# Performance work log

Measured on AMD Instinct MI355X. Metric: run time of the kernel, lower is better.

The kernel has to match this reference:

```python
import jax, jax.numpy as jnp
import numpy as np

SIGMA_INIT = 1000.0


def setup_inputs() -> dict:
    key = jax.random.key(0)
    k1, k2, k3 = jax.random.split(key, 3)
    B, M, D, S = 1024, 209, 12288, 2
    input_data = jax.random.normal(k1, (B, D), dtype=jnp.float32)
    center = jax.random.normal(k2, (M, D), dtype=jnp.float32)
    sigma = SIGMA_INIT * jnp.ones((M,), dtype=jnp.float32)
    W = 50.0 * jax.random.normal(k3, (S, M), dtype=jnp.float32)
    b = jnp.zeros((S,), dtype=jnp.float32)
    return {"input_data": input_data, "center": center, "sigma": sigma, "W": W, "b": b}


def reference(input_data, center, sigma, W, b):
    # Euclidean distance ||x_i - c_j|| via GEMM expansion (avoids [B,M,D] diff tensor)
    x2 = jnp.sum(input_data * input_data, axis=1, keepdims=True)        # [B,1]
    c2 = jnp.sum(center * center, axis=1)[None, :]                      # [1,M]
    d2 = x2 + c2 - 2.0 * (input_data @ center.T)                        # [B,M]
    dist = jnp.sqrt(jnp.maximum(d2, 0.0))
    # Note: original divides the (non-squared) norm by sigma^2, then exp(-.)
    radial = jnp.exp(-dist / (sigma * sigma)[None, :])                  # [B,M]
    return radial @ W.T + b                                             # [B,S]
```

## Files before the change

### kernel.cpp

```cpp
#include <hip/hip_runtime.h>
#include <hip/hip_bf16.h>
#include <stdint.h>

#define B_SZ 1024
#define M_SZ 209
#define MPAD 224
#define D_SZ 12288
#define KC   48
#define KCH  (D_SZ / KC)
#define BK   64
#define NIT  (KCH / BK)
#define NB   16
#define BT   64
#define NCT  14

#define CBF_OFF  0u
#define XXP_OFF  (MPAD * D_SZ * 2)
#define CC_OFF   (XXP_OFF + B_SZ * KC * 4)
#define SLAB_OFF (CC_OFF + 1024)

typedef __attribute__((ext_vector_type(8))) short short8;
typedef __attribute__((ext_vector_type(4))) float floatx4;

__device__ __forceinline__ uint32_t pk2(float lo, float hi) {
    union { __hip_bfloat162 h; uint32_t u; } cv;
    cv.h = __float22bfloat162_rn(float2{lo, hi});
    return cv.u;
}

__device__ __forceinline__ void gload_lds16(const void* g, void* l) {
    __builtin_amdgcn_global_load_lds(
        (const __attribute__((address_space(1))) void*)g,
        (__attribute__((address_space(3))) void*)l, 16, 0, 0);
}

__global__ __launch_bounds__(256) void rbf_prep(
    const float* __restrict__ c, unsigned short* __restrict__ cbf,
    float* __restrict__ cc)
{
    __shared__ float red[4];
    const int j = blockIdx.x, t = threadIdx.x;
    unsigned short* dst = cbf + (size_t)j * D_SZ;
    float s = 0.f;
    if (j < M_SZ) {
        const float* src = c + (size_t)j * D_SZ;
        for (int i = t * 4; i < D_SZ; i += 1024) {
            float4 v = *(const float4*)(src + i);
            s += v.x*v.x + v.y*v.y + v.z*v.z + v.w*v.w;
            uint2 w = { pk2(v.x, v.y), pk2(v.z, v.w) };
            *(uint2*)(dst + i) = w;
        }
    } else {
        uint2 zz = {0u, 0u};
        for (int i = t * 4; i < D_SZ; i += 1024) *(uint2*)(dst + i) = zz;
    }
#pragma unroll
    for (int off = 32; off > 0; off >>= 1) s += __shfl_down(s, off);
    if ((t & 63) == 0) red[t >> 6] = s;
    __syncthreads();
    if (t == 0 && j < M_SZ) cc[j] = red[0] + red[1] + red[2] + red[3];
}

__global__ __launch_bounds__(256, 3) void rbf_main(
    const float* __restrict__ x, const unsigned short* __restrict__ cbf,
    __hip_bfloat16* __restrict__ slab, float* __restrict__ xxp)
{
    __shared__ unsigned short sx[BT * BK];
    __shared__ unsigned short sc[MPAD * BK];

    const int t    = threadIdx.x;
    const int k    = blockIdx.x;
    const int b    = blockIdx.y;
    const int wave = t >> 6, lane = t & 63;
    const int quad = lane >> 4, mrow = lane & 15;
    const int m3   = mrow & 7;

    floatx4 acc[NCT];
    const floatx4 z4 = {0.f, 0.f, 0.f, 0.f};
#pragma unroll
    for (int i = 0; i < NCT; ++i) acc[i] = z4;

    const int r  = t >> 2;
    const int c0 = (t & 3) * 2;
    const float* xp = x + (size_t)(b * BT + r) * D_SZ + (size_t)k * KCH + (t & 3) * 16;
    unsigned short* xw0 = &sx[r * BK + ((c0    ) ^ (r & 7)) * 8];
    unsigned short* xw1 = &sx[r * BK + ((c0 + 1) ^ (r & 7)) * 8];

    const int lr8 = lane >> 3, lc8 = lane & 7;
    const unsigned short* cpb = cbf + (size_t)lr8 * D_SZ + (size_t)k * KCH
                              + (size_t)((lc8 ^ lr8) * 8);

    const unsigned short* ax0 = &sx[(wave * 16 + mrow) * BK + ((quad    ) ^ m3) * 8];
    const unsigned short* ax1 = &sx[(wave * 16 + mrow) * BK + ((quad + 4) ^ m3) * 8];
    const unsigned short* bx0 = &sc[mrow * BK + ((quad    ) ^ m3) * 8];
    const unsigned short* bx1 = &sc[mrow * BK + ((quad + 4) ^ m3) * 8];

    float sxx = 0.f;

    for (int it = 0; it < NIT; ++it) {
#pragma unroll
        for (int j = 0; j < 7; ++j) {
            const int cr = wave * 7 + j;
            gload_lds16(cpb + (size_t)cr * 8 * D_SZ + it * BK, &sc[cr * 512]);
        }
        {
            float4 v0 = *(const float4*)(xp + 0);
            float4 v1 = *(const float4*)(xp + 4);
            float4 v2 = *(const float4*)(xp + 8);
            float4 v3 = *(const float4*)(xp + 12);
            sxx += v0.x*v0.x + v0.y*v0.y + v0.z*v0.z + v0.w*v0.w
                 + v1.x*v1.x + v1.y*v1.y + v1.z*v1.z + v1.w*v1.w
                 + v2.x*v2.x + v2.y*v2.y + v2.z*v2.z + v2.w*v2.w
                 + v3.x*v3.x + v3.y*v3.y + v3.z*v3.z + v3.w*v3.w;
            uint4 w0 = { pk2(v0.x,v0.y), pk2(v0.z,v0.w), pk2(v1.x,v1.y), pk2(v1.z,v1.w) };
            uint4 w1 = { pk2(v2.x,v2.y), pk2(v2.z,v2.w), pk2(v3.x,v3.y), pk2(v3.z,v3.w) };
            *(uint4*)xw0 = w0;
            *(uint4*)xw1 = w1;
        }
        __syncthreads();

#pragma unroll
        for (int ks = 0; ks < 2; ++ks) {
            short8 a = *(const short8*)(ks ? ax1 : ax0);
            const unsigned short* bb = ks ? bx1 : bx0;
#pragma unroll
            for (int ct = 0; ct < NCT; ++ct) {
                short8 bf = *(const short8*)(bb + ct * 1024);
                acc[ct] = __builtin_amdgcn_mfma_f32_16x16x32_bf16(a, bf, acc[ct], 0, 0, 0);
            }
        }
        __syncthreads();
        xp += BK;
    }

    __hip_bfloat16* sd = slab + (size_t)k * B_SZ * M_SZ;
    const int gi0 = b * BT + wave * 16 + quad * 4;
#pragma unroll
    for (int ct = 0; ct < NCT; ++ct) {
        const int gj = ct * 16 + mrow;
        if (gj < M_SZ) {
#pragma unroll
            for (int rg = 0; rg < 4; ++rg)
                sd[(size_t)(gi0 + rg) * M_SZ + gj] = __float2bfloat16(acc[ct][rg]);
        }
    }

    sxx += __shfl_down(sxx, 2);
    sxx += __shfl_down(sxx, 1);
    if ((t & 3) == 0) xxp[(size_t)(b * BT + r) * KC + k] = sxx;
}

__global__ __launch_bounds__(256) void rbf_fin(
    const __hip_bfloat16* __restrict__ slab, const float* __restrict__ xxp,
    const float* __restrict__ cc, const float* __restrict__ sigma,
    const float* __restrict__ W, const float* __restrict__ bias,
    float* __restrict__ out)
{
    const int wave = threadIdx.x >> 6, lane = threadIdx.x & 63;
    const int i = blockIdx.x * 4 + wave;

    float xv = (lane < KC) ? xxp[(size_t)i * KC + lane] : 0.f;
#pragma unroll
    for (int off = 32; off > 0; off >>= 1) xv += __shfl_down(xv, off);
    const float xxi = __shfl(xv, 0);

    float a0 = 0.f, a1 = 0.f;
    for (int j = lane; j < M_SZ; j += 64) {
        float s = 0.f;
#pragma unroll
        for (int kk = 0; kk < KC; ++kk)
            s += __bfloat162float(slab[(size_t)kk * B_SZ * M_SZ + (size_t)i * M_SZ + j]);
        float d2 = fmaxf(xxi + cc[j] - 2.f * s, 0.f);
        float sg = sigma[j];
        float rad = __expf(-sqrtf(d2) / (sg * sg));
        a0 += rad * W[j];
        a1 += rad * W[M_SZ + j];
    }
#pragma unroll
    for (int off = 32; off > 0; off >>= 1) {
        a0 += __shfl_down(a0, off);
        a1 += __shfl_down(a1, off);
    }
    if (lane == 0) {
        out[i * 2 + 0] = a0 + bias[0];
        out[i * 2 + 1] = a1 + bias[1];
    }
}

extern "C" void kernel_launch(void* const* d_in, const int* in_sizes, int n_in,
                              void* d_out, int out_size, void* d_ws, size_t ws_size,
                              hipStream_t stream)
{
    const float* x     = (const float*)d_in[0];
    const float* c     = (const float*)d_in[1];
    const float* sigma = (const float*)d_in[2];
    const float* W     = (const float*)d_in[3];
    const float* bias  = (const float*)d_in[4];
    float* out = (float*)d_out;

    char* ws = (char*)d_ws;
    unsigned short*  cbf  = (unsigned short*)(ws + CBF_OFF);
    float*           xxp  = (float*)(ws + XXP_OFF);
    float*           cc   = (float*)(ws + CC_OFF);
    __hip_bfloat16*  slab = (__hip_bfloat16*)(ws + SLAB_OFF);

    rbf_prep<<<MPAD, 256, 0, stream>>>(c, cbf, cc);
    rbf_main<<<dim3(KC, NB), 256, 0, stream>>>(x, cbf, slab, xxp);
    rbf_fin<<<B_SZ / 4, 256, 0, stream>>>(slab, xxp, cc, sigma, W, bias, out);
}
```

Baseline: 119.1 us.

## Relayout partial-sum slab per row and vectorize split-K reduction

The split-K partial slab is stored so that each row's 48 partial chunks sit together (row stride KC*256), which lets the final kernel read 16-byte vectors and reduce across K in a block-per-row layout with shared-memory partials. The main kernel now prefetches all of its x tile (4 iterations) into registers before the K loop, so global load latency no longer stalls inside the loop. The prep kernel switches to 16-byte stores. The cost is higher register pressure in the main kernel and a slab that includes the padded columns.

```diff
diff --git a/kernel.cpp b/kernel.cpp
--- a/kernel.cpp
+++ b/kernel.cpp
@@ -13,6 +13,8 @@
 #define NB   16
 #define BT   64
 #define NCT  14
+#define SROW 256
+#define SLROW (KC * SROW)
 
 #define CBF_OFF  0u
 #define XXP_OFF  (MPAD * D_SZ * 2)
@@ -26,6 +28,12 @@
     union { __hip_bfloat162 h; uint32_t u; } cv;
     cv.h = __float22bfloat162_rn(float2{lo, hi});
     return cv.u;
+}
+
+__device__ __forceinline__ float bfbits2f(unsigned short u) {
+    union { uint32_t u; float f; } cv;
+    cv.u = ((uint32_t)u) << 16;
+    return cv.f;
 }
 
 __device__ __forceinline__ void gload_lds16(const void* g, void* l) {
@@ -44,15 +52,17 @@
     float s = 0.f;
     if (j < M_SZ) {
         const float* src = c + (size_t)j * D_SZ;
-        for (int i = t * 4; i < D_SZ; i += 1024) {
-            float4 v = *(const float4*)(src + i);
-            s += v.x*v.x + v.y*v.y + v.z*v.z + v.w*v.w;
-            uint2 w = { pk2(v.x, v.y), pk2(v.z, v.w) };
-            *(uint2*)(dst + i) = w;
+        for (int i = t * 8; i < D_SZ; i += 2048) {
+            float4 v0 = *(const float4*)(src + i);
+            float4 v1 = *(const float4*)(src + i + 4);
+            s += v0.x*v0.x + v0.y*v0.y + v0.z*v0.z + v0.w*v0.w
+               + v1.x*v1.x + v1.y*v1.y + v1.z*v1.z + v1.w*v1.w;
+            uint4 w = { pk2(v0.x,v0.y), pk2(v0.z,v0.w), pk2(v1.x,v1.y), pk2(v1.z,v1.w) };
+            *(uint4*)(dst + i) = w;
         }
     } else {
-        uint2 zz = {0u, 0u};
-        for (int i = t * 4; i < D_SZ; i += 1024) *(uint2*)(dst + i) = zz;
+        uint4 zz = {0u, 0u, 0u, 0u};
+        for (int i = t * 8; i < D_SZ; i += 2048) *(uint4*)(dst + i) = zz;
     }
 #pragma unroll
     for (int off = 32; off > 0; off >>= 1) s += __shfl_down(s, off);
@@ -83,6 +93,23 @@
     const int r  = t >> 2;
     const int c0 = (t & 3) * 2;
     const float* xp = x + (size_t)(b * BT + r) * D_SZ + (size_t)k * KCH + (t & 3) * 16;
+
+    uint4 xw[NIT][2];
+    float sxx = 0.f;
+#pragma unroll
+    for (int it = 0; it < NIT; ++it) {
+        float4 v0 = *(const float4*)(xp + it * BK + 0);
+        float4 v1 = *(const float4*)(xp + it * BK + 4);
+        float4 v2 = *(const float4*)(xp + it * BK + 8);
+        float4 v3 = *(const float4*)(xp + it * BK + 12);
+        sxx += v0.x*v0.x + v0.y*v0.y + v0.z*v0.z + v0.w*v0.w
+             + v1.x*v1.x + v1.y*v1.y + v1.z*v1.z + v1.w*v1.w
+             + v2.x*v2.x + v2.y*v2.y + v2.z*v2.z + v2.w*v2.w
+             + v3.x*v3.x + v3.y*v3.y + v3.z*v3.z + v3.w*v3.w;
+        xw[it][0] = make_uint4(pk2(v0.x,v0.y), pk2(v0.z,v0.w), pk2(v1.x,v1.y), pk2(v1.z,v1.w));
+        xw[it][1] = make_uint4(pk2(v2.x,v2.y), pk2(v2.z,v2.w), pk2(v3.x,v3.y), pk2(v3.z,v3.w));
+    }
+
     unsigned short* xw0 = &sx[r * BK + ((c0    ) ^ (r & 7)) * 8];
     unsigned short* xw1 = &sx[r * BK + ((c0 + 1) ^ (r & 7)) * 8];
 
@@ -95,28 +122,14 @@
     const unsigned short* bx0 = &sc[mrow * BK + ((quad    ) ^ m3) * 8];
     const unsigned short* bx1 = &sc[mrow * BK + ((quad + 4) ^ m3) * 8];
 
-    float sxx = 0.f;
-
     for (int it = 0; it < NIT; ++it) {
 #pragma unroll
         for (int j = 0; j < 7; ++j) {
             const int cr = wave * 7 + j;
             gload_lds16(cpb + (size_t)cr * 8 * D_SZ + it * BK, &sc[cr * 512]);
         }
-        {
-            float4 v0 = *(const float4*)(xp + 0);
-            float4 v1 = *(const float4*)(xp + 4);
-            float4 v2 = *(const float4*)(xp + 8);
-            float4 v3 = *(const float4*)(xp + 12);
-            sxx += v0.x*v0.x + v0.y*v0.y + v0.z*v0.z + v0.w*v0.w
-                 + v1.x*v1.x + v1.y*v1.y + v1.z*v1.z + v1.w*v1.w
-                 + v2.x*v2.x + v2.y*v2.y + v2.z*v2.z + v2.w*v2.w
-                 + v3.x*v3.x + v3.y*v3.y + v3.z*v3.z + v3.w*v3.w;
-            uint4 w0 = { pk2(v0.x,v0.y), pk2(v0.z,v0.w), pk2(v1.x,v1.y), pk2(v1.z,v1.w) };
-            uint4 w1 = { pk2(v2.x,v2.y), pk2(v2.z,v2.w), pk2(v3.x,v3.y), pk2(v3.z,v3.w) };
-            *(uint4*)xw0 = w0;
-            *(uint4*)xw1 = w1;
-        }
+        *(uint4*)xw0 = xw[it][0];
+        *(uint4*)xw1 = xw[it][1];
         __syncthreads();
 
 #pragma unroll
@@ -130,19 +143,16 @@
             }
         }
         __syncthreads();
-        xp += BK;
-    }
-
-    __hip_bfloat16* sd = slab + (size_t)k * B_SZ * M_SZ;
+    }
+
+    __hip_bfloat16* sd = slab + (size_t)k * SROW;
     const int gi0 = b * BT + wave * 16 + quad * 4;
 #pragma unroll
     for (int ct = 0; ct < NCT; ++ct) {
         const int gj = ct * 16 + mrow;
-        if (gj < M_SZ) {
-#pragma unroll
-            for (int rg = 0; rg < 4; ++rg)
-                sd[(size_t)(gi0 + rg) * M_SZ + gj] = __float2bfloat16(acc[ct][rg]);
-        }
+#pragma unroll
+        for (int rg = 0; rg < 4; ++rg)
+            sd[(size_t)(gi0 + rg) * SLROW + gj] = __float2bfloat16(acc[ct][rg]);
     }
 
     sxx += __shfl_down(sxx, 2);
@@ -156,34 +166,62 @@
     const float* __restrict__ W, const float* __restrict__ bias,
     float* __restrict__ out)
 {
-    const int wave = threadIdx.x >> 6, lane = threadIdx.x & 63;
-    const int i = blockIdx.x * 4 + wave;
-
-    float xv = (lane < KC) ? xxp[(size_t)i * KC + lane] : 0.f;
-#pragma unroll
-    for (int off = 32; off > 0; off >>= 1) xv += __shfl_down(xv, off);
-    const float xxi = __shfl(xv, 0);
-
-    float a0 = 0.f, a1 = 0.f;
-    for (int j = lane; j < M_SZ; j += 64) {
-        float s = 0.f;
-#pragma unroll
-        for (int kk = 0; kk < KC; ++kk)
-            s += __bfloat162float(slab[(size_t)kk * B_SZ * M_SZ + (size_t)i * M_SZ + j]);
-        float d2 = fmaxf(xxi + cc[j] - 2.f * s, 0.f);
-        float sg = sigma[j];
-        float rad = __expf(-sqrtf(d2) / (sg * sg));
-        a0 += rad * W[j];
-        a1 += rad * W[M_SZ + j];
-    }
-#pragma unroll
-    for (int off = 32; off > 0; off >>= 1) {
-        a0 += __shfl_down(a0, off);
-        a1 += __shfl_down(a1, off);
-    }
-    if (lane == 0) {
-        out[i * 2 + 0] = a0 + bias[0];
-        out[i * 2 + 1] = a1 + bias[1];
+    __shared__ float jpart[MPAD * 9];
+    __shared__ float jtot[MPAD];
+    __shared__ float xsh;
+
+    const int t = threadIdx.x;
+    const int i = blockIdx.x;
+
+    if (t < 64) {
+        float xv = (t < KC) ? xxp[(size_t)i * KC + t] : 0.f;
+#pragma unroll
+        for (int off = 32; off > 0; off >>= 1) xv += __shfl_down(xv, off);
+        if (t == 0) xsh = xv;
+    }
+
+    const int o = t % 28, g = t / 28;
+    if (t < 252) {
+        const unsigned short* sp = (const unsigned short*)slab
+                                 + (size_t)i * SLROW + o * 8;
+        float s8[8] = {0.f,0.f,0.f,0.f,0.f,0.f,0.f,0.f};
+        for (int kk = g; kk < KC; kk += 9) {
+            short8 v = *(const short8*)(sp + kk * SROW);
+#pragma unroll
+            for (int e = 0; e < 8; ++e) s8[e] += bfbits2f((unsigned short)v[e]);
+        }
+#pragma unroll
+        for (int e = 0; e < 8; ++e) jpart[(o * 8 + e) * 9 + g] = s8[e];
+    }
+    __syncthreads();
+
+    if (t < MPAD) {
+        float d = 0.f;
+#pragma unroll
+        for (int g2 = 0; g2 < 9; ++g2) d += jpart[t * 9 + g2];
+        jtot[t] = d;
+    }
+    __syncthreads();
+
+    if (t < 64) {
+        const float xxi = xsh;
+        float a0 = 0.f, a1 = 0.f;
+        for (int j = t; j < M_SZ; j += 64) {
+            float d2 = fmaxf(xxi + cc[j] - 2.f * jtot[j], 0.f);
+            float sg = sigma[j];
+            float rad = __expf(-sqrtf(d2) / (sg * sg));
+            a0 += rad * W[j];
+            a1 += rad * W[M_SZ + j];
+        }
+#pragma unroll
+        for (int off = 32; off > 0; off >>= 1) {
+            a0 += __shfl_down(a0, off);
+            a1 += __shfl_down(a1, off);
+        }
+        if (t == 0) {
+            out[i * 2 + 0] = a0 + bias[0];
+            out[i * 2 + 1] = a1 + bias[1];
+        }
     }
 }
 
@@ -206,5 +244,5 @@
 
     rbf_prep<<<MPAD, 256, 0, stream>>>(c, cbf, cc);
     rbf_main<<<dim3(KC, NB), 256, 0, stream>>>(x, cbf, slab, xxp);
-    rbf_fin<<<B_SZ / 4, 256, 0, stream>>>(slab, xxp, cc, sigma, W, bias, out);
-}
+    rbf_fin<<<B_SZ, 256, 0, stream>>>(slab, xxp, cc, sigma, W, bias, out);
+}
```

Result: faster. 113.6 us (-4.6%).
